# Optimization experiments

Measured on AMD Instinct MI355X. Metric: run time of the kernel, lower is better.

## Reference

```python
import jax, jax.numpy as jnp
import numpy as np

N_NODES = 50000
N_EDGES = 600000
N_GRAPHS = 512
DIM = 128
N_FEAT = 78
N_LAYERS = 4
BN_EPS = 1e-5


def setup_inputs() -> dict:
    key = jax.random.key(0)
    ks = jax.random.split(key, 12)
    w = lambda k, s: (jax.random.normal(k, s, jnp.float32) * 0.05)
    x = jax.random.normal(ks[0], (N_NODES, N_FEAT), jnp.float32)
    edge_index = jax.random.randint(ks[1], (2, N_EDGES), 0, N_NODES)
    batch = jnp.sort(jax.random.randint(ks[2], (N_NODES,), 0, N_GRAPHS))
    return {
        "x": x,
        "edge_index": edge_index,
        "batch": batch,
        "ini_w1": w(ks[3], (N_FEAT, DIM)),
        "ini_b1": jnp.zeros((DIM,), jnp.float32),
        "ini_w2": w(ks[4], (DIM, DIM)),
        "ini_b2": jnp.zeros((DIM,), jnp.float32),
        "gin_w1": w(ks[5], (N_LAYERS, DIM, DIM)),
        "gin_b1": jnp.zeros((N_LAYERS, DIM), jnp.float32),
        "gin_w2": w(ks[6], (N_LAYERS, DIM, DIM)),
        "gin_b2": jnp.zeros((N_LAYERS, DIM), jnp.float32),
        "bn_gamma": jnp.ones((N_LAYERS, DIM), jnp.float32),
        "bn_beta": jnp.zeros((N_LAYERS, DIM), jnp.float32),
        "layer_w": w(ks[7], (N_LAYERS,)),  # Conv2d(L,1,(1,1)) weight
        "layer_b": jnp.zeros((1,), jnp.float32),
    }


def reference(x, edge_index, batch, ini_w1, ini_b1, ini_w2, ini_b2,
              gin_w1, gin_b1, gin_w2, gin_b2, bn_gamma, bn_beta,
              layer_w, layer_b):
    # ini_embed: Linear -> ReLU -> Linear
    h = jnp.maximum(x @ ini_w1 + ini_b1, 0.0) @ ini_w2 + ini_b2  # [N, D]
    src, dst = edge_index[0], edge_index[1]
    embeds = []
    for i in range(N_LAYERS):
        # GINConv (eps=0): mlp(x_i + sum_{j->i} x_j)
        agg = jax.ops.segment_sum(h[src], dst, num_segments=N_NODES)
        z = h + agg
        z = jnp.maximum(z @ gin_w1[i] + gin_b1[i], 0.0) @ gin_w2[i] + gin_b2[i]
        z = jnp.maximum(z, 0.0)  # F.relu after conv
        # BatchNorm1d (training mode: batch stats, biased var)
        mean = jnp.mean(z, axis=0)
        var = jnp.mean((z - mean) ** 2, axis=0)
        h = (z - mean) * jax.lax.rsqrt(var + BN_EPS) * bn_gamma[i] + bn_beta[i]
        embeds.append(h)
    layer_nodes = jnp.stack(embeds, axis=1)  # [N, L, D]
    # layer_conv Conv2d(L,1,(1,1)): learned weighted sum over layer axis + bias
    pos_global_node = jnp.einsum('nld,l->nd', layer_nodes, layer_w) + layer_b
    # global_add_pool over graphs
    pos_global_graph = jax.ops.segment_sum(pos_global_node, batch,
                                           num_segments=N_GRAPHS)  # [G, D]
    return pos_global_graph
```

## Files before the change

kernel.cpp:

```cpp
#include <hip/hip_runtime.h>

#define N_NODES  50000
#define N_EDGES  600000
#define N_GRAPHS 512
#define DIM      128
#define N_FEAT   78
#define N_LAYERS 4
#define BN_EPS   1e-5f
#define SLOT_CAP 64
#define LDA      136
#define NPART    16

#define NBKT     196
#define NBLK_BIN 128
#define BCAP     64
#define EDGES_PER_BIN ((N_EDGES + NBLK_BIN - 1) / NBLK_BIN)

#define GSTART_BLOCKS 196
#define ZERO_BLOCKS 512
#define GBLOCKS ((N_NODES + 63) / 64)
#define TW_ELEMS (10 * 16384)
#define BN_FLOATS (N_LAYERS * NPART * 256)

typedef __attribute__((ext_vector_type(8))) _Float16 f16x8;
typedef __attribute__((ext_vector_type(4))) float f32x4;

static __device__ __forceinline__ short f2h(float f) {
    _Float16 h = (_Float16)f;
    union { _Float16 h; short s; } u; u.h = h;
    return u.s;
}
static __device__ __forceinline__ float h2f(ushort s) {
    union { ushort s; _Float16 h; } u; u.s = s;
    return (float)u.h;
}


__global__ __launch_bounds__(256) void transpose_weights(const float* __restrict__ ini_w1,
                                                         const float* __restrict__ ini_w2,
                                                         const float* __restrict__ gw1,
                                                         const float* __restrict__ gw2,
                                                         short* __restrict__ wt,
                                                         float* __restrict__ bnstat) {
    int gid = blockIdx.x * 256 + threadIdx.x;
    if (gid < TW_ELEMS) {
        int m = gid >> 14;
        int idx = gid & 16383;
        int n = idx >> 7;
        int k = idx & 127;
        const float* src;
        int K = 128;
        if (m == 0) { src = ini_w1; K = N_FEAT; }
        else if (m == 1) src = ini_w2;
        else if (m < 6) src = gw1 + (m - 2) * 16384;
        else src = gw2 + (m - 6) * 16384;
        float v = (k < K) ? src[k * 128 + n] : 0.f;
        wt[m * 16384 + n * 128 + k] = f2h(v);
    } else {
        int bi = gid - TW_ELEMS;
        if (bi < BN_FLOATS) bnstat[bi] = 0.0f;
    }
}


__global__ __launch_bounds__(256, 4) void ini_fused(const float* __restrict__ x,
                                                    const short* __restrict__ Wt1,
                                                    const float* __restrict__ b1,
                                                    const short* __restrict__ Wt2,
                                                    const float* __restrict__ b2,
                                                    ushort* __restrict__ Cout,
                                                    const int* __restrict__ src,
                                                    const int* __restrict__ dst,
                                                    const int* __restrict__ batch,
                                                    int* __restrict__ bcnt,
                                                    uint* __restrict__ bpool,
                                                    int* __restrict__ gstart,
                                                    float* __restrict__ gsum,
                                                    float* __restrict__ gssq) {
    __shared__ short As[64 * LDA];
    __shared__ short Bs[64 * LDA];
    int tid = threadIdx.x;

    if (blockIdx.x >= GBLOCKS) {
        int b = blockIdx.x - GBLOCKS;
        if (b < NBLK_BIN) {
            int* lcur = (int*)As;
            for (int i = tid; i < NBKT; i += 256) lcur[i] = 0;
            __syncthreads();
            int base = b * EDGES_PER_BIN;
            int lim = min(base + EDGES_PER_BIN, N_EDGES);
            for (int e = base + tid; e < lim; e += 256) {
                int d = dst[e];
                int s = src[e];
                int bk = d >> 8;
                int p = atomicAdd(&lcur[bk], 1);
                if (p < BCAP)
                    bpool[(bk * NBLK_BIN + b) * BCAP + p] =
                        ((uint)(d & 255) << 16) | (uint)s;
            }
            __syncthreads();
            for (int i = tid; i < NBKT; i += 256) bcnt[b * NBKT + i] = lcur[i];
            return;
        }
        b -= NBLK_BIN;
        if (b < GSTART_BLOCKS) {
            int n = b * 256 + tid;
            if (n < N_NODES) {
                int g = batch[n];
                int gp = (n == 0) ? -1 : batch[n - 1];
                for (int gg = gp + 1; gg <= g; ++gg) gstart[gg] = n;
                if (n == N_NODES - 1)
                    for (int gg = g + 1; gg <= N_GRAPHS; ++gg) gstart[gg] = N_NODES;
            }
            return;
        }
        b -= GSTART_BLOCKS;
        float4 z = make_float4(0.f, 0.f, 0.f, 0.f);
        float* bse = (b < 256) ? gsum : gssq;
        int off = (b & 255) * 1024 + tid * 4;
        *(float4*)&bse[off] = z;
        return;
    }

    int row0 = blockIdx.x * 64;
    int wave = tid >> 6;
    int wlane = tid & 63;
    int rw = wave >> 1;
    int cw = wave & 1;
    int lm = wlane & 15;
    int quad = wlane >> 4;
    const int wrow = (cw * 64 + lm) * 128 + quad * 8;

    f16x8 bcur[4], bnxt[4];
    #pragma unroll
    for (int nt = 0; nt < 4; ++nt)
        bcur[nt] = *(const f16x8*)&Wt1[wrow + nt * 2048];

    #pragma unroll
    for (int j = 0; j < 32; ++j) {
        int lin = tid + j * 256;
        int r = lin >> 7;
        int k = lin & 127;
        int gr = row0 + r;
        float v = 0.f;
        if (gr < N_NODES && k < N_FEAT) v = x[gr * N_FEAT + k];
        As[r * LDA + k] = f2h(v);
    }
    __syncthreads();

    f32x4 acc[2][4];
    #pragma unroll
    for (int mt = 0; mt < 2; ++mt)
        #pragma unroll
        for (int nt = 0; nt < 4; ++nt)
            acc[mt][nt] = (f32x4){0.f, 0.f, 0.f, 0.f};

    #pragma unroll
    for (int ks = 0; ks < 4; ++ks) {
        if (ks < 3) {
            #pragma unroll
            for (int nt = 0; nt < 4; ++nt)
                bnxt[nt] = *(const f16x8*)&Wt1[wrow + nt * 2048 + (ks + 1) * 32];
        }
        int kb = ks * 32 + quad * 8;
        f16x8 a0 = *(const f16x8*)&As[(rw * 32 + lm) * LDA + kb];
        f16x8 a1 = *(const f16x8*)&As[(rw * 32 + 16 + lm) * LDA + kb];
        #pragma unroll
        for (int nt = 0; nt < 4; ++nt) {
            acc[0][nt] = __builtin_amdgcn_mfma_f32_16x16x32_f16(a0, bcur[nt], acc[0][nt], 0, 0, 0);
            acc[1][nt] = __builtin_amdgcn_mfma_f32_16x16x32_f16(a1, bcur[nt], acc[1][nt], 0, 0, 0);
        }
        #pragma unroll
        for (int nt = 0; nt < 4; ++nt) bcur[nt] = bnxt[nt];
    }

    #pragma unroll
    for (int nt = 0; nt < 4; ++nt) {
        int col = cw * 64 + nt * 16 + lm;
        float bv = b1[col];
        #pragma unroll
        for (int mt = 0; mt < 2; ++mt) {
            #pragma unroll
            for (int r = 0; r < 4; ++r) {
                int row = rw * 32 + mt * 16 + quad * 4 + r;
                Bs[row * LDA + col] = (short)f2h(fmaxf(acc[mt][nt][r] + bv, 0.f));
            }
        }
    }
    #pragma unroll
    for (int nt = 0; nt < 4; ++nt)
        bcur[nt] = *(const f16x8*)&Wt2[wrow + nt * 2048];
    __syncthreads();

    #pragma unroll
    for (int mt = 0; mt < 2; ++mt)
        #pragma unroll
        for (int nt = 0; nt < 4; ++nt)
            acc[mt][nt] = (f32x4){0.f, 0.f, 0.f, 0.f};
    #pragma unroll
    for (int ks = 0; ks < 4; ++ks) {
        if (ks < 3) {
            #pragma unroll
            for (int nt = 0; nt < 4; ++nt)
                bnxt[nt] = *(const f16x8*)&Wt2[wrow + nt * 2048 + (ks + 1) * 32];
        }
        int kb = ks * 32 + quad * 8;
        f16x8 a0 = *(const f16x8*)&Bs[(rw * 32 + lm) * LDA + kb];
        f16x8 a1 = *(const f16x8*)&Bs[(rw * 32 + 16 + lm) * LDA + kb];
        #pragma unroll
        for (int nt = 0; nt < 4; ++nt) {
            acc[0][nt] = __builtin_amdgcn_mfma_f32_16x16x32_f16(a0, bcur[nt], acc[0][nt], 0, 0, 0);
            acc[1][nt] = __builtin_amdgcn_mfma_f32_16x16x32_f16(a1, bcur[nt], acc[1][nt], 0, 0, 0);
        }
        #pragma unroll
        for (int nt = 0; nt < 4; ++nt) bcur[nt] = bnxt[nt];
    }

    ushort* Cs = (ushort*)As;
    #pragma unroll
    for (int nt = 0; nt < 4; ++nt) {
        int col = cw * 64 + nt * 16 + lm;
        float bv = b2[col];
        #pragma unroll
        for (int mt = 0; mt < 2; ++mt) {
            #pragma unroll
            for (int r = 0; r < 4; ++r) {
                int row = rw * 32 + mt * 16 + quad * 4 + r;
                Cs[row * LDA + col] = (ushort)f2h(acc[mt][nt][r] + bv);
            }
        }
    }
    __syncthreads();

    #pragma unroll
    for (int j = 0; j < 4; ++j) {
        int lin = tid + j * 256;
        int r = lin >> 4;
        int kc = lin & 15;
        int gr = row0 + r;
        if (gr < N_NODES)
            *(uint4*)&Cout[gr * 128 + kc * 8] = *(const uint4*)&Cs[r * LDA + kc * 8];
    }
}


__global__ __launch_bounds__(256) void build_slot(const uint* __restrict__ bpool,
                                                  const int* __restrict__ bcnt,
                                                  int* __restrict__ cnt,
                                                  ushort* __restrict__ slot) {
    __shared__ ushort lslot[256 * SLOT_CAP];
    __shared__ int lcnt[256];
    __shared__ int rcnt[NBLK_BIN];
    int tid = threadIdx.x;
    int bkt = blockIdx.x;
    lcnt[tid] = 0;
    if (tid < NBLK_BIN) rcnt[tid] = min(bcnt[tid * NBKT + bkt], BCAP);
    __syncthreads();
    const uint* pool = bpool + (size_t)bkt * NBLK_BIN * BCAP;
    #pragma unroll 1
    for (int i = tid; i < NBLK_BIN * BCAP; i += 256) {
        int run = i >> 6;
        int pos = i & (BCAP - 1);
        if (pos < rcnt[run]) {
            uint u = pool[i];
            int ls = u >> 16;
            int p = atomicAdd(&lcnt[ls], 1);
            if (p < SLOT_CAP) lslot[ls * SLOT_CAP + p] = (ushort)(u & 0xffffu);
        }
    }
    __syncthreads();
    int node0 = bkt << 8;
    int gn = node0 + tid;
    if (gn < N_NODES) cnt[gn] = lcnt[tid];
    #pragma unroll
    for (int j = 0; j < 8; ++j) {
        int i = tid + j * 256;
        int r = i >> 3;
        int c = i & 7;
        int g = node0 + r;
        if (g < N_NODES)
            *(uint4*)&slot[g * SLOT_CAP + c * 8] = *(const uint4*)&lslot[r * SLOT_CAP + c * 8];
    }
}


__global__ __launch_bounds__(256, 4) void gin_fused(const ushort* __restrict__ Z,
                                                    const int* __restrict__ cnt,
                                                    const ushort* __restrict__ slot,
                                                    const float* __restrict__ bnpart,
                                                    const float* __restrict__ gamma,
                                                    const float* __restrict__ beta,
                                                    const short* __restrict__ Wt1,
                                                    const float* __restrict__ b1,
                                                    const short* __restrict__ Wt2,
                                                    const float* __restrict__ b2,
                                                    ushort* __restrict__ C,
                                                    const int* __restrict__ batch,
                                                    float* __restrict__ gsum,
                                                    float* __restrict__ gssq,
                                                    float* __restrict__ bnpart_out) {
    __shared__ short As[64 * LDA];
    __shared__ short Bs[64 * LDA];
    __shared__ float saff[128], taff[128];
    __shared__ float scr[256];
    __shared__ int sb[64];
    int tid = threadIdx.x;
    int row0 = blockIdx.x * 64;

    int wave = tid >> 6;
    int wlane = tid & 63;
    int rw = wave >> 1;
    int cw = wave & 1;
    int lm = wlane & 15;
    int quad = wlane >> 4;
    const int wrow = (cw * 64 + lm) * 128 + quad * 8;

    if (tid < 128) {
        float s = 1.0f, t = 0.0f;
        if (bnpart) {
            float sum = 0.f, ssq = 0.f;
            #pragma unroll
            for (int p = 0; p < NPART; ++p) {
                sum += bnpart[p * 256 + tid];
                ssq += bnpart[p * 256 + 128 + tid];
            }
            const float invN = 1.0f / (float)N_NODES;
            float m = sum * invN;
            float var = ssq * invN - m * m;
            s = gamma[tid] * rsqrtf(var + BN_EPS);
            t = beta[tid] - m * s;
        }
        saff[tid] = s; taff[tid] = t;
    }
    if (tid < 64) {
        int n = row0 + tid;
        sb[tid] = (n < N_NODES) ? batch[n] : -1;
    }
    __syncthreads();

    {
        int lane = tid & 15;
        int nsub = tid >> 4;
        union U { uint4 u; _Float16 h[8]; };
        union I { uint4 u; ushort s[8]; };
        const uint4* z4 = (const uint4*)Z;
        #pragma unroll 1
        for (int pass = 0; pass < 4; ++pass) {
            int r = pass * 16 + nsub;
            int node = row0 + r;
            float v[8];
            float dsc = 1.0f;
            if (node < N_NODES) {
                U zu; zu.u = z4[node * 16 + lane];
                #pragma unroll
                for (int j = 0; j < 8; ++j) v[j] = (float)zu.h[j];
                int dtrue = cnt[node];
                int d = min(dtrue, SLOT_CAP);
                const ushort* sl = slot + node * SLOT_CAP;
                int e = 0;
                for (; e + 8 <= d; e += 8) {
                    I si; si.u = *(const uint4*)&sl[e];
                    U u[8];
                    #pragma unroll
                    for (int q = 0; q < 8; ++q) u[q].u = z4[(int)si.s[q] * 16 + lane];
                    #pragma unroll
                    for (int j = 0; j < 8; ++j) {
                        float a = ((float)u[0].h[j] + (float)u[1].h[j]) +
                                  ((float)u[2].h[j] + (float)u[3].h[j]);
                        float b = ((float)u[4].h[j] + (float)u[5].h[j]) +
                                  ((float)u[6].h[j] + (float)u[7].h[j]);
                        v[j] += a + b;
                    }
                }
                if (e + 4 <= d) {
                    int s0 = sl[e], s1 = sl[e + 1], s2 = sl[e + 2], s3 = sl[e + 3];
                    U u0, u1, u2, u3;
                    u0.u = z4[s0 * 16 + lane];
                    u1.u = z4[s1 * 16 + lane];
                    u2.u = z4[s2 * 16 + lane];
                    u3.u = z4[s3 * 16 + lane];
                    #pragma unroll
                    for (int j = 0; j < 8; ++j)
                        v[j] += ((float)u0.h[j] + (float)u1.h[j]) +
                                ((float)u2.h[j] + (float)u3.h[j]);
                    e += 4;
                }
                for (; e < d; ++e) {
                    U u; u.u = z4[(int)sl[e] * 16 + lane];
                    #pragma unroll
                    for (int j = 0; j < 8; ++j) v[j] += (float)u.h[j];
                }
                dsc = 1.0f + (float)dtrue;
            } else {
                #pragma unroll
                for (int j = 0; j < 8; ++j) v[j] = 0.f;
                dsc = 0.f;
            }
            #pragma unroll
            for (int j = 0; j < 8; ++j) {
                int dd = lane * 8 + j;
                As[r * LDA + dd] = f2h(saff[dd] * v[j] + dsc * taff[dd]);
            }
        }
    }

    f16x8 bcur[4], bnxt[4];
    #pragma unroll
    for (int nt = 0; nt < 4; ++nt)
        bcur[nt] = *(const f16x8*)&Wt1[wrow + nt * 2048];
    __syncthreads();

    f32x4 acc[2][4];
    #pragma unroll
    for (int mt = 0; mt < 2; ++mt)
        #pragma unroll
        for (int nt = 0; nt < 4; ++nt)
            acc[mt][nt] = (f32x4){0.f, 0.f, 0.f, 0.f};
    #pragma unroll
    for (int ks = 0; ks < 4; ++ks) {
        if (ks < 3) {
            #pragma unroll
            for (int nt = 0; nt < 4; ++nt)
                bnxt[nt] = *(const f16x8*)&Wt1[wrow + nt * 2048 + (ks + 1) * 32];
        }
        int kb = ks * 32 + quad * 8;
        f16x8 a0 = *(const f16x8*)&As[(rw * 32 + lm) * LDA + kb];
        f16x8 a1 = *(const f16x8*)&As[(rw * 32 + 16 + lm) * LDA + kb];
        #pragma unroll
        for (int nt = 0; nt < 4; ++nt) {
            acc[0][nt] = __builtin_amdgcn_mfma_f32_16x16x32_f16(a0, bcur[nt], acc[0][nt], 0, 0, 0);
            acc[1][nt] = __builtin_amdgcn_mfma_f32_16x16x32_f16(a1, bcur[nt], acc[1][nt], 0, 0, 0);
        }
        #pragma unroll
        for (int nt = 0; nt < 4; ++nt) bcur[nt] = bnxt[nt];
    }
    #pragma unroll
    for (int nt = 0; nt < 4; ++nt) {
        int col = cw * 64 + nt * 16 + lm;
        float bv = b1[col];
        #pragma unroll
        for (int mt = 0; mt < 2; ++mt) {
            #pragma unroll
            for (int r = 0; r < 4; ++r) {
                int row = rw * 32 + mt * 16 + quad * 4 + r;
                Bs[row * LDA + col] = (short)f2h(fmaxf(acc[mt][nt][r] + bv, 0.f));
            }
        }
    }
    #pragma unroll
    for (int nt = 0; nt < 4; ++nt)
        bcur[nt] = *(const f16x8*)&Wt2[wrow + nt * 2048];
    __syncthreads();

    #pragma unroll
    for (int mt = 0; mt < 2; ++mt)
        #pragma unroll
        for (int nt = 0; nt < 4; ++nt)
            acc[mt][nt] = (f32x4){0.f, 0.f, 0.f, 0.f};
    #pragma unroll
    for (int ks = 0; ks < 4; ++ks) {
        if (ks < 3) {
            #pragma unroll
            for (int nt = 0; nt < 4; ++nt)
                bnxt[nt] = *(const f16x8*)&Wt2[wrow + nt * 2048 + (ks + 1) * 32];
        }
        int kb = ks * 32 + quad * 8;
        f16x8 c0 = *(const f16x8*)&Bs[(rw * 32 + lm) * LDA + kb];
        f16x8 c1 = *(const f16x8*)&Bs[(rw * 32 + 16 + lm) * LDA + kb];
        #pragma unroll
        for (int nt = 0; nt < 4; ++nt) {
            acc[0][nt] = __builtin_amdgcn_mfma_f32_16x16x32_f16(c0, bcur[nt], acc[0][nt], 0, 0, 0);
            acc[1][nt] = __builtin_amdgcn_mfma_f32_16x16x32_f16(c1, bcur[nt], acc[1][nt], 0, 0, 0);
        }
        #pragma unroll
        for (int nt = 0; nt < 4; ++nt) bcur[nt] = bnxt[nt];
    }
    ushort* Cs = (ushort*)As;
    #pragma unroll
    for (int nt = 0; nt < 4; ++nt) {
        int col = cw * 64 + nt * 16 + lm;
        float bv = b2[col];
        #pragma unroll
        for (int mt = 0; mt < 2; ++mt) {
            #pragma unroll
            for (int r = 0; r < 4; ++r) {
                int row = rw * 32 + mt * 16 + quad * 4 + r;
                Cs[row * LDA + col] = (ushort)f2h(fmaxf(acc[mt][nt][r] + bv, 0.f));
            }
        }
    }
    __syncthreads();

    #pragma unroll
    for (int j = 0; j < 4; ++j) {
        int lin = tid + j * 256;
        int r = lin >> 4;
        int kc = lin & 15;
        int gr = row0 + r;
        if (gr < N_NODES)
            *(uint4*)&C[gr * 128 + kc * 8] = *(const uint4*)&Cs[r * LDA + kc * 8];
    }

    {
        int c = tid & 127;
        int rbase = (tid >> 7) * 32;
        int curg = sb[rbase];
        float rs = 0.f, rss = 0.f;
        float ts = 0.f, tss = 0.f;
        for (int r = rbase; r < rbase + 32; ++r) {
            int g = sb[r];
            if (g < 0) break;
            if (g != curg) {
                atomicAdd(&gsum[curg * 128 + c], rs);
                atomicAdd(&gssq[curg * 128 + c], rss);
                rs = 0.f; rss = 0.f; curg = g;
            }
            float v = h2f(Cs[r * LDA + c]);
            rs += v; rss += v * v;
            ts += v; tss += v * v;
        }
        if (curg >= 0) {
            atomicAdd(&gsum[curg * 128 + c], rs);
            atomicAdd(&gssq[curg * 128 + c], rss);
        }
        if (tid >= 128) { scr[c] = ts; scr[128 + c] = tss; }
        __syncthreads();
        if (tid < 128) {
            float* part = bnpart_out + (blockIdx.x & (NPART - 1)) * 256;
            atomicAdd(&part[c], ts + scr[c]);
            atomicAdd(&part[128 + c], tss + scr[128 + c]);
        }
    }
}


__global__ __launch_bounds__(256) void combine(const float* __restrict__ gsum,
                                               const float* __restrict__ bnstat,
                                               const int* __restrict__ gstart,
                                               const float* __restrict__ gamma,
                                               const float* __restrict__ beta,
                                               const float* __restrict__ LW,
                                               const float* __restrict__ LB,
                                               float* __restrict__ out) {
    int gid = blockIdx.x * 256 + threadIdx.x;
    if (gid >= N_GRAPHS * 128) return;
    int g = gid >> 7;
    int d = gid & 127;
    float c = (float)(gstart[g + 1] - gstart[g]);
    float o = c * LB[0];
    const float invN = 1.0f / (float)N_NODES;
    #pragma unroll
    for (int l = 0; l < N_LAYERS; ++l) {
        const float* part = bnstat + l * NPART * 256;
        float sum = 0.f, ssq = 0.f;
        #pragma unroll
        for (int p = 0; p < NPART; ++p) {
            sum += part[p * 256 + d];
            ssq += part[p * 256 + 128 + d];
        }
        float m = sum * invN;
        float var = ssq * invN - m * m;
        float s = gamma[l * 128 + d] * rsqrtf(var + BN_EPS);
        float t = beta[l * 128 + d] - m * s;
        o += LW[l] * (s * gsum[(l * N_GRAPHS + g) * 128 + d] + c * t);
    }
    out[gid] = o;
}


extern "C" void kernel_launch(void* const* d_in, const int* in_sizes, int n_in,
                              void* d_out, int out_size, void* d_ws, size_t ws_size,
                              hipStream_t stream) {
    const float* x      = (const float*)d_in[0];
    const int*   ei     = (const int*)d_in[1];
    const int*   batch  = (const int*)d_in[2];
    const float* ini_w1 = (const float*)d_in[3];
    const float* ini_b1 = (const float*)d_in[4];
    const float* ini_w2 = (const float*)d_in[5];
    const float* ini_b2 = (const float*)d_in[6];
    const float* gw1    = (const float*)d_in[7];
    const float* gb1    = (const float*)d_in[8];
    const float* gw2    = (const float*)d_in[9];
    const float* gb2    = (const float*)d_in[10];
    const float* gamma  = (const float*)d_in[11];
    const float* beta   = (const float*)d_in[12];
    const float* lw     = (const float*)d_in[13];
    const float* lb     = (const float*)d_in[14];
    float* out = (float*)d_out;

    char* p = (char*)d_ws;
    auto carve = [&](size_t bytes) -> char* {
        char* q = p;
        p += (bytes + 255) & ~(size_t)255;
        return q;
    };
    ushort* z0    = (ushort*)carve(sizeof(ushort) * N_NODES * DIM);
    ushort* z1    = (ushort*)carve(sizeof(ushort) * N_NODES * DIM);
    float* bnstat = (float*)carve(sizeof(float) * BN_FLOATS);
    float* gsum   = (float*)carve(sizeof(float) * N_LAYERS * N_GRAPHS * DIM);
    float* gssq   = (float*)carve(sizeof(float) * N_LAYERS * N_GRAPHS * DIM);
    short* wbf    = (short*)carve(sizeof(short) * 10 * 128 * 128);
    int* gstart   = (int*)carve(sizeof(int) * (N_GRAPHS + 1));
    int* cnt      = (int*)carve(sizeof(int) * N_NODES);
    ushort* slot  = (ushort*)carve(sizeof(ushort) * N_NODES * SLOT_CAP);
    int* bcnt     = (int*)carve(sizeof(int) * NBLK_BIN * NBKT);
    uint* bpool   = (uint*)carve(sizeof(uint) * NBKT * NBLK_BIN * BCAP);

    const int* src = ei;
    const int* dst = ei + N_EDGES;

    int twblocks = (TW_ELEMS + BN_FLOATS + 255) / 256;
    transpose_weights<<<twblocks, 256, 0, stream>>>(
        ini_w1, ini_w2, gw1, gw2, wbf, bnstat);

    ini_fused<<<GBLOCKS + NBLK_BIN + GSTART_BLOCKS + ZERO_BLOCKS, 256, 0, stream>>>(
        x, wbf, ini_b1, wbf + 16384, ini_b2, z0,
        src, dst, batch, bcnt, bpool, gstart, gsum, gssq);

    build_slot<<<NBKT, 256, 0, stream>>>(bpool, bcnt, cnt, slot);

    ushort* zprev = z0;
    ushort* znext = z1;
    for (int i = 0; i < N_LAYERS; ++i) {
        const float* bp_in = (i == 0) ? nullptr : bnstat + (i - 1) * NPART * 256;
        const float* gptr  = (i == 0) ? gamma : gamma + (i - 1) * DIM;
        const float* bptr  = (i == 0) ? beta : beta + (i - 1) * DIM;
        gin_fused<<<GBLOCKS, 256, 0, stream>>>(
            zprev, cnt, slot, bp_in, gptr, bptr,
            wbf + (2 + i) * 16384, gb1 + i * DIM,
            wbf + (6 + i) * 16384, gb2 + i * DIM, znext, batch,
            gsum + i * N_GRAPHS * DIM, gssq + i * N_GRAPHS * DIM,
            bnstat + i * NPART * 256);
        ushort* tmp = zprev; zprev = znext; znext = tmp;
    }
    combine<<<(N_GRAPHS * 128 + 255) / 256, 256, 0, stream>>>(
        gsum, bnstat, gstart, gamma, beta, lw, lb, out);
}
```

Before: 317.6 us.

## Regroup prep stages: fold binning into prep, build slots alongside initial MLP

Result: slower. 339.6 us (+6.9%).

```diff
diff --git a/kernel.cpp b/kernel.cpp
--- a/kernel.cpp
+++ b/kernel.cpp
@@ -21,6 +21,7 @@
 #define GBLOCKS ((N_NODES + 63) / 64)
 #define TW_ELEMS (10 * 16384)
 #define BN_FLOATS (N_LAYERS * NPART * 256)
+#define TWB ((TW_ELEMS + BN_FLOATS + 255) / 256)
 
 typedef __attribute__((ext_vector_type(8))) _Float16 f16x8;
 typedef __attribute__((ext_vector_type(4))) float f32x4;
@@ -36,30 +37,80 @@
 }
 
 
-__global__ __launch_bounds__(256) void transpose_weights(const float* __restrict__ ini_w1,
-                                                         const float* __restrict__ ini_w2,
-                                                         const float* __restrict__ gw1,
-                                                         const float* __restrict__ gw2,
-                                                         short* __restrict__ wt,
-                                                         float* __restrict__ bnstat) {
-    int gid = blockIdx.x * 256 + threadIdx.x;
-    if (gid < TW_ELEMS) {
-        int m = gid >> 14;
-        int idx = gid & 16383;
-        int n = idx >> 7;
-        int k = idx & 127;
-        const float* src;
-        int K = 128;
-        if (m == 0) { src = ini_w1; K = N_FEAT; }
-        else if (m == 1) src = ini_w2;
-        else if (m < 6) src = gw1 + (m - 2) * 16384;
-        else src = gw2 + (m - 6) * 16384;
-        float v = (k < K) ? src[k * 128 + n] : 0.f;
-        wt[m * 16384 + n * 128 + k] = f2h(v);
-    } else {
-        int bi = gid - TW_ELEMS;
-        if (bi < BN_FLOATS) bnstat[bi] = 0.0f;
-    }
+__global__ __launch_bounds__(256) void prep(const float* __restrict__ ini_w1,
+                                            const float* __restrict__ ini_w2,
+                                            const float* __restrict__ gw1,
+                                            const float* __restrict__ gw2,
+                                            short* __restrict__ wt,
+                                            float* __restrict__ bnstat,
+                                            const int* __restrict__ src,
+                                            const int* __restrict__ dst,
+                                            const int* __restrict__ batch,
+                                            int* __restrict__ bcnt,
+                                            uint* __restrict__ bpool,
+                                            int* __restrict__ gstart,
+                                            float* __restrict__ gsum,
+                                            float* __restrict__ gssq) {
+    __shared__ int lcur[NBKT];
+    int tid = threadIdx.x;
+    int b = blockIdx.x;
+    if (b < TWB) {
+        int gid = b * 256 + tid;
+        if (gid < TW_ELEMS) {
+            int m = gid >> 14;
+            int idx = gid & 16383;
+            int n = idx >> 7;
+            int k = idx & 127;
+            const float* s;
+            int K = 128;
+            if (m == 0) { s = ini_w1; K = N_FEAT; }
+            else if (m == 1) s = ini_w2;
+            else if (m < 6) s = gw1 + (m - 2) * 16384;
+            else s = gw2 + (m - 6) * 16384;
+            float v = (k < K) ? s[k * 128 + n] : 0.f;
+            wt[m * 16384 + n * 128 + k] = f2h(v);
+        } else {
+            int bi = gid - TW_ELEMS;
+            if (bi < BN_FLOATS) bnstat[bi] = 0.0f;
+        }
+        return;
+    }
+    b -= TWB;
+    if (b < NBLK_BIN) {
+        for (int i = tid; i < NBKT; i += 256) lcur[i] = 0;
+        __syncthreads();
+        int base = b * EDGES_PER_BIN;
+        int lim = min(base + EDGES_PER_BIN, N_EDGES);
+        for (int e = base + tid; e < lim; e += 256) {
+            int d = dst[e];
+            int s = src[e];
+            int bk = d >> 8;
+            int p = atomicAdd(&lcur[bk], 1);
+            if (p < BCAP)
+                bpool[(bk * NBLK_BIN + b) * BCAP + p] =
+                    ((uint)(d & 255) << 16) | (uint)s;
+        }
+        __syncthreads();
+        for (int i = tid; i < NBKT; i += 256) bcnt[b * NBKT + i] = lcur[i];
+        return;
+    }
+    b -= NBLK_BIN;
+    if (b < GSTART_BLOCKS) {
+        int n = b * 256 + tid;
+        if (n < N_NODES) {
+            int g = batch[n];
+            int gp = (n == 0) ? -1 : batch[n - 1];
+            for (int gg = gp + 1; gg <= g; ++gg) gstart[gg] = n;
+            if (n == N_NODES - 1)
+                for (int gg = g + 1; gg <= N_GRAPHS; ++gg) gstart[gg] = N_NODES;
+        }
+        return;
+    }
+    b -= GSTART_BLOCKS;
+    float4 z = make_float4(0.f, 0.f, 0.f, 0.f);
+    float* bse = (b < 256) ? gsum : gssq;
+    int off = (b & 255) * 1024 + tid * 4;
+    *(float4*)&bse[off] = z;
 }
 
 
@@ -69,59 +120,62 @@
                                                     const short* __restrict__ Wt2,
                                                     const float* __restrict__ b2,
                                                     ushort* __restrict__ Cout,
-                                                    const int* __restrict__ src,
-                                                    const int* __restrict__ dst,
-                                                    const int* __restrict__ batch,
-                                                    int* __restrict__ bcnt,
-                                                    uint* __restrict__ bpool,
-                                                    int* __restrict__ gstart,
-                                                    float* __restrict__ gsum,
-                                                    float* __restrict__ gssq) {
-    __shared__ short As[64 * LDA];
-    __shared__ short Bs[64 * LDA];
+                                                    const uint* __restrict__ bpool,
+                                                    const int* __restrict__ bcnt,
+                                                    int* __restrict__ cnt,
+                                                    ushort* __restrict__ slot) {
+    __shared__ short smem[2 * 64 * LDA];
     int tid = threadIdx.x;
 
     if (blockIdx.x >= GBLOCKS) {
-        int b = blockIdx.x - GBLOCKS;
-        if (b < NBLK_BIN) {
-            int* lcur = (int*)As;
-            for (int i = tid; i < NBKT; i += 256) lcur[i] = 0;
-            __syncthreads();
-            int base = b * EDGES_PER_BIN;
-            int lim = min(base + EDGES_PER_BIN, N_EDGES);
-            for (int e = base + tid; e < lim; e += 256) {
-                int d = dst[e];
-                int s = src[e];
-                int bk = d >> 8;
-                int p = atomicAdd(&lcur[bk], 1);
-                if (p < BCAP)
-                    bpool[(bk * NBLK_BIN + b) * BCAP + p] =
-                        ((uint)(d & 255) << 16) | (uint)s;
-            }
-            __syncthreads();
-            for (int i = tid; i < NBKT; i += 256) bcnt[b * NBKT + i] = lcur[i];
-            return;
-        }
-        b -= NBLK_BIN;
-        if (b < GSTART_BLOCKS) {
-            int n = b * 256 + tid;
-            if (n < N_NODES) {
-                int g = batch[n];
-                int gp = (n == 0) ? -1 : batch[n - 1];
-                for (int gg = gp + 1; gg <= g; ++gg) gstart[gg] = n;
-                if (n == N_NODES - 1)
-                    for (int gg = g + 1; gg <= N_GRAPHS; ++gg) gstart[gg] = N_NODES;
-            }
-            return;
-        }
-        b -= GSTART_BLOCKS;
-        float4 z = make_float4(0.f, 0.f, 0.f, 0.f);
-        float* bse = (b < 256) ? gsum : gssq;
-        int off = (b & 255) * 1024 + tid * 4;
-        *(float4*)&bse[off] = z;
+        int bkt = blockIdx.x - GBLOCKS;
+        ushort* lslot = (ushort*)smem;
+        int* lcnt = (int*)((char*)smem + 32768);
+        int* rcnt = (int*)((char*)smem + 33792);
+        lcnt[tid] = 0;
+        if (tid < NBLK_BIN) rcnt[tid] = min(bcnt[tid * NBKT + bkt], BCAP);
+        __syncthreads();
+        const uint* pool = bpool + (size_t)bkt * NBLK_BIN * BCAP;
+        #pragma unroll 1
+        for (int i = tid; i < NBLK_BIN * BCAP; i += 256) {
+            int run = i >> 6;
+            int pos = i & (BCAP - 1);
+            if (pos < rcnt[run]) {
+                uint u = pool[i];
+                int ls = u >> 16;
+                int p = atomicAdd(&lcnt[ls], 1);
+                if (p < SLOT_CAP) lslot[ls * SLOT_CAP + p] = (ushort)(u & 0xffffu);
+            }
+        }
+        __syncthreads();
+        {
+            int n2 = min(lcnt[tid], SLOT_CAP);
+            ushort* L = lslot + tid * SLOT_CAP;
+            for (int i = 1; i < n2; ++i) {
+                ushort key = L[i];
+                int j = i - 1;
+                while (j >= 0 && L[j] > key) { L[j + 1] = L[j]; --j; }
+                L[j + 1] = key;
+            }
+        }
+        __syncthreads();
+        int node0 = bkt << 8;
+        int gn = node0 + tid;
+        if (gn < N_NODES) cnt[gn] = lcnt[tid];
+        #pragma unroll
+        for (int j = 0; j < 8; ++j) {
+            int i = tid + j * 256;
+            int r = i >> 3;
+            int c = i & 7;
+            int g = node0 + r;
+            if (g < N_NODES)
+                *(uint4*)&slot[g * SLOT_CAP + c * 8] = *(const uint4*)&lslot[r * SLOT_CAP + c * 8];
+        }
         return;
     }
 
+    short* As = smem;
+    short* Bs = smem + 64 * LDA;
     int row0 = blockIdx.x * 64;
     int wave = tid >> 6;
     int wlane = tid & 63;
@@ -136,15 +190,40 @@
     for (int nt = 0; nt < 4; ++nt)
         bcur[nt] = *(const f16x8*)&Wt1[wrow + nt * 2048];
 
-    #pragma unroll
-    for (int j = 0; j < 32; ++j) {
-        int lin = tid + j * 256;
-        int r = lin >> 7;
-        int k = lin & 127;
-        int gr = row0 + r;
-        float v = 0.f;
-        if (gr < N_NODES && k < N_FEAT) v = x[gr * N_FEAT + k];
-        As[r * LDA + k] = f2h(v);
+    for (int i = tid; i < 64 * 25; i += 256) {
+        int r = i / 25, c = i % 25;
+        *(uint*)&As[r * LDA + 78 + c * 2] = 0u;
+    }
+    if (row0 + 64 <= N_NODES) {
+        const float* xb = x + (size_t)row0 * N_FEAT;
+        #pragma unroll
+        for (int q = 0; q < 5; ++q) {
+            int idx = tid + q * 256;
+            if (idx < 1248) {
+                float4 f4 = ((const float4*)xb)[idx];
+                int f0 = idx * 4;
+                As[(f0 / 78) * LDA + (f0 % 78)] = f2h(f4.x);
+                int f1 = f0 + 1;
+                As[(f1 / 78) * LDA + (f1 % 78)] = f2h(f4.y);
+                int f2 = f0 + 2;
+                As[(f2 / 78) * LDA + (f2 % 78)] = f2h(f4.z);
+                int f3 = f0 + 3;
+                As[(f3 / 78) * LDA + (f3 % 78)] = f2h(f4.w);
+            }
+        }
+    } else {
+        #pragma unroll
+        for (int j = 0; j < 32; ++j) {
+            int lin = tid + j * 256;
+            int r = lin >> 7;
+            int k = lin & 127;
+            int gr = row0 + r;
+            if (k < N_FEAT) {
+                float v = 0.f;
+                if (gr < N_NODES) v = x[gr * N_FEAT + k];
+                As[r * LDA + k] = f2h(v);
+            }
+        }
     }
     __syncthreads();
 
@@ -240,46 +319,6 @@
         int gr = row0 + r;
         if (gr < N_NODES)
             *(uint4*)&Cout[gr * 128 + kc * 8] = *(const uint4*)&Cs[r * LDA + kc * 8];
-    }
-}
-
-
-__global__ __launch_bounds__(256) void build_slot(const uint* __restrict__ bpool,
-                                                  const int* __restrict__ bcnt,
-                                                  int* __restrict__ cnt,
-                                                  ushort* __restrict__ slot) {
-    __shared__ ushort lslot[256 * SLOT_CAP];
-    __shared__ int lcnt[256];
-    __shared__ int rcnt[NBLK_BIN];
-    int tid = threadIdx.x;
-    int bkt = blockIdx.x;
-    lcnt[tid] = 0;
-    if (tid < NBLK_BIN) rcnt[tid] = min(bcnt[tid * NBKT + bkt], BCAP);
-    __syncthreads();
-    const uint* pool = bpool + (size_t)bkt * NBLK_BIN * BCAP;
-    #pragma unroll 1
-    for (int i = tid; i < NBLK_BIN * BCAP; i += 256) {
-        int run = i >> 6;
-        int pos = i & (BCAP - 1);
-        if (pos < rcnt[run]) {
-            uint u = pool[i];
-            int ls = u >> 16;
-            int p = atomicAdd(&lcnt[ls], 1);
-            if (p < SLOT_CAP) lslot[ls * SLOT_CAP + p] = (ushort)(u & 0xffffu);
-        }
-    }
-    __syncthreads();
-    int node0 = bkt << 8;
-    int gn = node0 + tid;
-    if (gn < N_NODES) cnt[gn] = lcnt[tid];
-    #pragma unroll
-    for (int j = 0; j < 8; ++j) {
-        int i = tid + j * 256;
-        int r = i >> 3;
-        int c = i & 7;
-        int g = node0 + r;
-        if (g < N_NODES)
-            *(uint4*)&slot[g * SLOT_CAP + c * 8] = *(const uint4*)&lslot[r * SLOT_CAP + c * 8];
     }
 }
 
@@ -609,15 +648,13 @@
     const int* src = ei;
     const int* dst = ei + N_EDGES;
 
-    int twblocks = (TW_ELEMS + BN_FLOATS + 255) / 256;
-    transpose_weights<<<twblocks, 256, 0, stream>>>(
-        ini_w1, ini_w2, gw1, gw2, wbf, bnstat);
-
-    ini_fused<<<GBLOCKS + NBLK_BIN + GSTART_BLOCKS + ZERO_BLOCKS, 256, 0, stream>>>(
+    prep<<<TWB + NBLK_BIN + GSTART_BLOCKS + ZERO_BLOCKS, 256, 0, stream>>>(
+        ini_w1, ini_w2, gw1, gw2, wbf, bnstat,
+        src, dst, batch, bcnt, bpool, gstart, gsum, gssq);
+
+    ini_fused<<<GBLOCKS + NBKT, 256, 0, stream>>>(
         x, wbf, ini_b1, wbf + 16384, ini_b2, z0,
-        src, dst, batch, bcnt, bpool, gstart, gsum, gssq);
-
-    build_slot<<<NBKT, 256, 0, stream>>>(bpool, bcnt, cnt, slot);
+        bpool, bcnt, cnt, slot);
 
     ushort* zprev = z0;
     ushort* znext = z1;
```
